# Performance work log

Hardware: AMD Instinct MI355X
Metric: run time of the kernel (lower is better)

Reference implementation:

```python
import jax, jax.numpy as jnp
import numpy as np

NUM_TOKENS = 8192
EMBED_DIM = 32
BETA = 1.0
DECAY = 0.99
L2_EPS = 1e-12  # torch F.normalize denom clamp


def l2norm(t):
    return t / jnp.maximum(jnp.linalg.norm(t, axis=-1, keepdims=True), L2_EPS)


def setup_inputs() -> dict:
    key = jax.random.key(0)
    k1, k2 = jax.random.split(key)
    z = jax.random.normal(k1, (32, EMBED_DIM, 16, 16), dtype=jnp.float32)  # [B, C, H, W]
    embedding = l2norm(jax.random.normal(k2, (NUM_TOKENS, EMBED_DIM), dtype=jnp.float32))
    cluster_sizes = jnp.zeros((NUM_TOKENS,), dtype=jnp.float32)
    return {"z": z, "embedding": embedding, "cluster_sizes": cluster_sizes}


def reference(z, embedding, cluster_sizes):
    B, C, H, W = z.shape
    zc = jnp.transpose(z, (0, 2, 3, 1))          # channel_last: [B, H, W, C]
    zn = l2norm(zc)
    z_flat = zn.reshape(-1, C)                   # [N, C], N = B*H*W

    # nearest centroid by cosine similarity (codebook rows are unit norm)
    cos_sim = z_flat @ embedding.T               # [N, K]
    token_ids = jnp.argmax(cos_sim, axis=-1)     # [N]
    z_q_flat = embedding[token_ids]              # gather, [N, C]
    z_q = z_q_flat.reshape(zn.shape)

    # EMA statistics (training branch; one-hot @ matmuls expressed as scatter-adds)
    bins = jnp.zeros((NUM_TOKENS,), z.dtype).at[token_ids].add(1.0)      # encodings.sum(0)
    new_cluster_sizes = cluster_sizes * DECAY + (1.0 - DECAY) * bins
    zero_mask = bins == 0
    bins_c = jnp.where(zero_mask, 1.0, bins)
    embed_sum = jnp.zeros((NUM_TOKENS, C), z.dtype).at[token_ids].add(z_flat)  # (z_flat.T @ onehot).T
    embed_normalized = l2norm(embed_sum / bins_c[:, None])
    embed_normalized = jnp.where(zero_mask[:, None], embedding, embed_normalized)
    new_embedding = l2norm(embedding * DECAY + (1.0 - DECAY) * embed_normalized)

    # commitment loss + straight-through estimator
    loss = BETA * jnp.mean((jax.lax.stop_gradient(z_q) - zn) ** 2)
    z_q_st = zn + jax.lax.stop_gradient(z_q - zn)
    z_q_out = jnp.transpose(z_q_st, (0, 3, 1, 2))  # back to [B, C, H, W]

    return (z_q_out, loss, token_ids.reshape(B, H, W), new_embedding, new_cluster_sizes)
```

## Files before the change

kernel.cpp:

```cpp
#include <hip/hip_runtime.h>


#define NTOK   8192
#define NCODE  8192
#define CDIM   32
#define HW     256
#define DECAYF 0.99f
#define EPSF   0.01f

#define OUT_ZQ   0
#define OUT_LOSS 262144
#define OUT_IDS  262145
#define OUT_EMB  270337
#define OUT_CS   532481

#define WS_ZN     0u
#define WS_ZNBF   1048576u
#define WS_EBF    1572864u
#define WS_PMAX   2097152u
#define WS_PACK   3145728u

#define CHUNK  256
#define NCHUNK (NCODE / CHUNK)
#define TILES  (CHUNK / 16)

typedef __attribute__((ext_vector_type(8))) short bf16x8;
typedef __attribute__((ext_vector_type(4))) float f32x4;

__device__ inline unsigned short f2bf(float x) {
    unsigned u = __float_as_uint(x);
    return (unsigned short)((u + 0x7FFFu + ((u >> 16) & 1u)) >> 16);
}
__device__ inline unsigned fmap(float s) {
    unsigned u = __float_as_uint(s);
    return (u & 0x80000000u) ? ~u : (u | 0x80000000u);
}

__device__ inline void stage_chunk(const unsigned short* __restrict__ ebf,
                                   int kbase, float4* lbs5, int t) {
    const float4* src = (const float4*)(ebf + (size_t)kbase * CDIM);
#pragma unroll
    for (int j = 0; j < 4; ++j) {
        int u = t + j * 256;
        int row = u >> 2, seg = u & 3;
        lbs5[row * 5 + seg] = src[u];
    }
}

__global__ __launch_bounds__(256) void k_prep(const float* __restrict__ z,
                                              const float* __restrict__ emb,
                                              float* __restrict__ zn,
                                              unsigned short* __restrict__ znbf,
                                              unsigned short* __restrict__ ebf,
                                              unsigned long long* __restrict__ packed,
                                              float* __restrict__ out) {
    int bid = blockIdx.x, t = threadIdx.x;
    if (bid < 32) {
        int n = bid * 256 + t;
        int b = n >> 8, hw = n & 255;
        const float* zp = z + (size_t)b * (CDIM * HW) + hw;
        float v[CDIM];
        float ss = 0.f;
#pragma unroll
        for (int c = 0; c < CDIM; ++c) {
            float tv = zp[c * HW];
            v[c] = tv;
            ss += tv * tv;
        }
        float d = fmaxf(sqrtf(ss), 1e-12f);
        float* o = zn + (size_t)n * CDIM;
        unsigned short* ob = znbf + (size_t)n * CDIM;
#pragma unroll
        for (int c = 0; c < CDIM; ++c) {
            float tv = v[c] / d;
            o[c] = tv;
            ob[c] = f2bf(tv);
        }
    } else if (bid < 160) {
        int base = (bid - 32) * 2048 + t * 8;
        const float4* s = (const float4*)(emb + base);
        float4 x4 = s[0], y4 = s[1];
        ushort4 u0 = {f2bf(x4.x), f2bf(x4.y), f2bf(x4.z), f2bf(x4.w)};
        ushort4 u1 = {f2bf(y4.x), f2bf(y4.y), f2bf(y4.z), f2bf(y4.w)};
        *(ushort4*)(ebf + base) = u0;
        *(ushort4*)(ebf + base + 4) = u1;
    } else if (bid < 164) {
        int base = (bid - 160) * 2048 + t;
#pragma unroll
        for (int j = 0; j < 8; ++j) packed[base + j * 256] = 0ull;
    } else {
        if (t == 0) out[OUT_LOSS] = 0.f;
    }
}

__global__ __launch_bounds__(256) void k_max(const unsigned short* __restrict__ znbf,
                                             const unsigned short* __restrict__ ebf,
                                             float* __restrict__ pmax) {
    __shared__ float4 lbs5[CHUNK * 5];
    __shared__ float lmax[256];
    int kbase = blockIdx.y * CHUNK;
    stage_chunk(ebf, kbase, lbs5, threadIdx.x);
    __syncthreads();

    int wave = threadIdx.x >> 6, lane = threadIdx.x & 63;
    int col = lane & 15, quad = lane >> 4;
    int wtok = blockIdx.x * 256 + wave * 64;

    bf16x8 a[4];
#pragma unroll
    for (int f = 0; f < 4; ++f)
        a[f] = *(const bf16x8*)(znbf + (size_t)(wtok + f * 16 + col) * CDIM + quad * 8);

    const bf16x8* bl = (const bf16x8*)lbs5;
    const f32x4 zero4 = {0.f, 0.f, 0.f, 0.f};
    float m[4][4];
#pragma unroll
    for (int f = 0; f < 4; ++f)
#pragma unroll
        for (int r = 0; r < 4; ++r) m[f][r] = -1e30f;

    for (int t = 0; t < TILES; ++t) {
        bf16x8 b = bl[(t * 16 + col) * 5 + quad];
#pragma unroll
        for (int f = 0; f < 4; ++f) {
            f32x4 d = __builtin_amdgcn_mfma_f32_16x16x32_bf16(a[f], b, zero4, 0, 0, 0);
#pragma unroll
            for (int r = 0; r < 4; ++r) m[f][r] = fmaxf(m[f][r], d[r]);
        }
    }
#pragma unroll
    for (int f = 0; f < 4; ++f)
#pragma unroll
        for (int r = 0; r < 4; ++r) {
            float v = m[f][r];
#pragma unroll
            for (int s = 1; s < 16; s <<= 1) v = fmaxf(v, __shfl_xor(v, s));
            if (col == 0) lmax[wave * 64 + f * 16 + quad * 4 + r] = v;
        }
    __syncthreads();
    pmax[(size_t)blockIdx.y * NTOK + blockIdx.x * 256 + threadIdx.x] = lmax[threadIdx.x];
}

__global__ __launch_bounds__(256) void k_pick(const unsigned short* __restrict__ znbf,
                                              const unsigned short* __restrict__ ebf,
                                              const float* __restrict__ zn,
                                              const float* __restrict__ emb,
                                              const float* __restrict__ pmax,
                                              unsigned long long* __restrict__ packed) {
    __shared__ float4 lbs5[CHUNK * 5];
    __shared__ float lthr[256];
    int kbase = blockIdx.y * CHUNK;
    stage_chunk(ebf, kbase, lbs5, threadIdx.x);
    {
        int tok = blockIdx.x * 256 + threadIdx.x;
        float mx = -1e30f;
#pragma unroll
        for (int ch = 0; ch < NCHUNK; ++ch)
            mx = fmaxf(mx, pmax[(size_t)ch * NTOK + tok]);
        lthr[threadIdx.x] = mx - EPSF;
    }
    __syncthreads();

    int wave = threadIdx.x >> 6, lane = threadIdx.x & 63;
    int col = lane & 15, quad = lane >> 4;
    int wtok = blockIdx.x * 256 + wave * 64;

    bf16x8 a[4];
#pragma unroll
    for (int f = 0; f < 4; ++f)
        a[f] = *(const bf16x8*)(znbf + (size_t)(wtok + f * 16 + col) * CDIM + quad * 8);

    float thr[4][4];
#pragma unroll
    for (int f = 0; f < 4; ++f)
#pragma unroll
        for (int r = 0; r < 4; ++r)
            thr[f][r] = lthr[wave * 64 + f * 16 + quad * 4 + r];

    const bf16x8* bl = (const bf16x8*)lbs5;
    const f32x4 zero4 = {0.f, 0.f, 0.f, 0.f};

    for (int t = 0; t < TILES; ++t) {
        bf16x8 b = bl[(t * 16 + col) * 5 + quad];
#pragma unroll
        for (int f = 0; f < 4; ++f) {
            f32x4 d = __builtin_amdgcn_mfma_f32_16x16x32_bf16(a[f], b, zero4, 0, 0, 0);
#pragma unroll
            for (int r = 0; r < 4; ++r) {
                if (d[r] >= thr[f][r]) {
                    int tok = wtok + f * 16 + quad * 4 + r;
                    int code = kbase + t * 16 + col;
                    const float* zp = zn + (size_t)tok * CDIM;
                    const float* ep = emb + (size_t)code * CDIM;
                    float a0 = 0.f, a1 = 0.f, a2 = 0.f, a3 = 0.f;
#pragma unroll
                    for (int j = 0; j < 8; ++j) {
                        a0 = __builtin_fmaf(zp[4 * j + 0], ep[4 * j + 0], a0);
                        a1 = __builtin_fmaf(zp[4 * j + 1], ep[4 * j + 1], a1);
                        a2 = __builtin_fmaf(zp[4 * j + 2], ep[4 * j + 2], a2);
                        a3 = __builtin_fmaf(zp[4 * j + 3], ep[4 * j + 3], a3);
                    }
                    float s = (a0 + a1) + (a2 + a3);
                    atomicMax(packed + tok, ((unsigned long long)fmap(s) << 13) |
                                            (unsigned long long)(8191 - code));
                }
            }
        }
    }
}

__global__ __launch_bounds__(256) void k_final(const unsigned long long* __restrict__ packed,
                                               const float* __restrict__ zn,
                                               const float* __restrict__ emb,
                                               const float* __restrict__ cs,
                                               float* __restrict__ out) {
    __shared__ float lesum[32][32];
    __shared__ int lbins[32];
    __shared__ int lsid[32];
    __shared__ float ls4[4];

    int blk = blockIdx.x, t = threadIdx.x;
    int wave = t >> 6, lane = t & 63;
    int tok0 = blk * 32, kbase = blk * 32;

    if (t < 32) lbins[t] = 0;
#pragma unroll
    for (int i = 0; i < 4; ++i) {
        int idx = i * 256 + t;
        lesum[idx >> 5][idx & 31] = 0.f;
    }
    if (t < 32) {
        int n = tok0 + t;
        int id = 8191 - (int)(packed[n] & 8191ull);
        lsid[t] = id;
        out[OUT_IDS + n] = (float)id;
    }
    __syncthreads();

    float s = 0.f;
#pragma unroll
    for (int i = 0; i < 4; ++i) {
        int idx = i * 256 + t;
        int tl = idx >> 5, c = idx & 31;
        int n = tok0 + tl;
        int id = lsid[tl];
        float ev = emb[(size_t)id * CDIM + c];
        float zv = zn[(size_t)n * CDIM + c];
        int b = n >> 8, hw = n & 255;
        out[OUT_ZQ + ((size_t)b * CDIM + c) * HW + hw] = ev;
        float dd = ev - zv;
        s += dd * dd;
    }
#pragma unroll
    for (int off = 32; off > 0; off >>= 1) s += __shfl_down(s, off);
    if (lane == 0) ls4[wave] = s;
    __syncthreads();
    if (t == 0)
        atomicAdd(out + OUT_LOSS,
                  (ls4[0] + ls4[1] + ls4[2] + ls4[3]) * (1.0f / 262144.0f));

    for (int i = 0; i < 32; ++i) {
        int n = i * 256 + t;
        int id = 8191 - (int)(packed[n] & 8191ull);
        unsigned kl = (unsigned)(id - kbase);
        if (kl < 32u) {
            atomicAdd(&lbins[kl], 1);
            const float* zp = zn + (size_t)n * CDIM;
#pragma unroll
            for (int c = 0; c < CDIM; ++c)
                atomicAdd(&lesum[kl][c], zp[c]);
        }
    }
    __syncthreads();

#pragma unroll
    for (int i = 0; i < 4; ++i) {
        int idx = i * 256 + t;
        int kl = idx >> 5, c = idx & 31;
        int k = kbase + kl;
        int bi = lbins[kl];
        float bf = (float)bi;
        bool zero = (bi == 0);
        float tv = lesum[kl][c] / (zero ? 1.0f : bf);
        float ss = tv * tv;
#pragma unroll
        for (int sh = 1; sh < 32; sh <<= 1) ss += __shfl_xor(ss, sh);
        float d = fmaxf(sqrtf(ss), 1e-12f);
        float ew = emb[(size_t)k * CDIM + c];
        float en = zero ? ew : (tv / d);
        float w = ew * DECAYF + (1.0f - DECAYF) * en;
        float ss2 = w * w;
#pragma unroll
        for (int sh = 1; sh < 32; sh <<= 1) ss2 += __shfl_xor(ss2, sh);
        float d2 = fmaxf(sqrtf(ss2), 1e-12f);
        out[OUT_EMB + (size_t)k * CDIM + c] = w / d2;
        if (c == 0) out[OUT_CS + k] = cs[k] * DECAYF + (1.0f - DECAYF) * bf;
    }
}

extern "C" void kernel_launch(void* const* d_in, const int* in_sizes, int n_in,
                              void* d_out, int out_size, void* d_ws, size_t ws_size,
                              hipStream_t stream) {
    const float* z   = (const float*)d_in[0];
    const float* emb = (const float*)d_in[1];
    const float* cs  = (const float*)d_in[2];
    float* out = (float*)d_out;
    char* ws = (char*)d_ws;

    float* zn                  = (float*)(ws + WS_ZN);
    unsigned short* znbf       = (unsigned short*)(ws + WS_ZNBF);
    unsigned short* ebf        = (unsigned short*)(ws + WS_EBF);
    float* pmax                = (float*)(ws + WS_PMAX);
    unsigned long long* packed = (unsigned long long*)(ws + WS_PACK);

    k_prep<<<dim3(165), 256, 0, stream>>>(z, emb, zn, znbf, ebf, packed, out);
    k_max<<<dim3(NTOK / 256, NCHUNK), 256, 0, stream>>>(znbf, ebf, pmax);
    k_pick<<<dim3(NTOK / 256, NCHUNK), 256, 0, stream>>>(znbf, ebf, zn, emb, pmax, packed);
    k_final<<<dim3(256), 256, 0, stream>>>(packed, zn, emb, cs, out);
}
```

Before: 120.2 us.

## Rewrite pick kernel to rescore only tokens whose chunk max is near global max

```diff
diff --git a/kernel.cpp b/kernel.cpp
--- a/kernel.cpp
+++ b/kernel.cpp
@@ -141,71 +141,64 @@
     pmax[(size_t)blockIdx.y * NTOK + blockIdx.x * 256 + threadIdx.x] = lmax[threadIdx.x];
 }
 
-__global__ __launch_bounds__(256) void k_pick(const unsigned short* __restrict__ znbf,
-                                              const unsigned short* __restrict__ ebf,
-                                              const float* __restrict__ zn,
-                                              const float* __restrict__ emb,
-                                              const float* __restrict__ pmax,
-                                              unsigned long long* __restrict__ packed) {
-    __shared__ float4 lbs5[CHUNK * 5];
-    __shared__ float lthr[256];
-    int kbase = blockIdx.y * CHUNK;
-    stage_chunk(ebf, kbase, lbs5, threadIdx.x);
-    {
-        int tok = blockIdx.x * 256 + threadIdx.x;
-        float mx = -1e30f;
-#pragma unroll
-        for (int ch = 0; ch < NCHUNK; ++ch)
-            mx = fmaxf(mx, pmax[(size_t)ch * NTOK + tok]);
-        lthr[threadIdx.x] = mx - EPSF;
-    }
-    __syncthreads();
-
-    int wave = threadIdx.x >> 6, lane = threadIdx.x & 63;
-    int col = lane & 15, quad = lane >> 4;
-    int wtok = blockIdx.x * 256 + wave * 64;
-
-    bf16x8 a[4];
-#pragma unroll
-    for (int f = 0; f < 4; ++f)
-        a[f] = *(const bf16x8*)(znbf + (size_t)(wtok + f * 16 + col) * CDIM + quad * 8);
-
-    float thr[4][4];
-#pragma unroll
-    for (int f = 0; f < 4; ++f)
-#pragma unroll
-        for (int r = 0; r < 4; ++r)
-            thr[f][r] = lthr[wave * 64 + f * 16 + quad * 4 + r];
-
-    const bf16x8* bl = (const bf16x8*)lbs5;
-    const f32x4 zero4 = {0.f, 0.f, 0.f, 0.f};
-
-    for (int t = 0; t < TILES; ++t) {
-        bf16x8 b = bl[(t * 16 + col) * 5 + quad];
-#pragma unroll
-        for (int f = 0; f < 4; ++f) {
-            f32x4 d = __builtin_amdgcn_mfma_f32_16x16x32_bf16(a[f], b, zero4, 0, 0, 0);
-#pragma unroll
-            for (int r = 0; r < 4; ++r) {
-                if (d[r] >= thr[f][r]) {
-                    int tok = wtok + f * 16 + quad * 4 + r;
-                    int code = kbase + t * 16 + col;
-                    const float* zp = zn + (size_t)tok * CDIM;
-                    const float* ep = emb + (size_t)code * CDIM;
-                    float a0 = 0.f, a1 = 0.f, a2 = 0.f, a3 = 0.f;
-#pragma unroll
-                    for (int j = 0; j < 8; ++j) {
-                        a0 = __builtin_fmaf(zp[4 * j + 0], ep[4 * j + 0], a0);
-                        a1 = __builtin_fmaf(zp[4 * j + 1], ep[4 * j + 1], a1);
-                        a2 = __builtin_fmaf(zp[4 * j + 2], ep[4 * j + 2], a2);
-                        a3 = __builtin_fmaf(zp[4 * j + 3], ep[4 * j + 3], a3);
-                    }
-                    float s = (a0 + a1) + (a2 + a3);
-                    atomicMax(packed + tok, ((unsigned long long)fmap(s) << 13) |
-                                            (unsigned long long)(8191 - code));
-                }
-            }
-        }
+__global__ __launch_bounds__(256, 4) void k_pick(const float* __restrict__ zn,
+                                                 const float* __restrict__ emb,
+                                                 const float* __restrict__ pmax,
+                                                 unsigned long long* __restrict__ packed) {
+    __shared__ int qlist[256];
+    __shared__ int qcnt;
+    int t = threadIdx.x, lane = t & 63;
+    int x = blockIdx.x, y = blockIdx.y;
+    int code = y * CHUNK + t;
+
+    if (t == 0) qcnt = 0;
+
+    const float4* ef = (const float4*)(emb + (size_t)code * CDIM);
+    float4 e0 = ef[0], e1 = ef[1], e2 = ef[2], e3 = ef[3];
+    float4 e4 = ef[4], e5 = ef[5], e6 = ef[6], e7 = ef[7];
+
+    int tok = x * 256 + t;
+    float mx = -1e30f, pmy = -1e30f;
+#pragma unroll
+    for (int ch = 0; ch < NCHUNK; ++ch) {
+        float p = pmax[(size_t)ch * NTOK + tok];
+        if (ch == y) pmy = p;
+        mx = fmaxf(mx, p);
+    }
+    __syncthreads();
+    if (pmy >= mx - EPSF) qlist[atomicAdd(&qcnt, 1)] = t;
+    __syncthreads();
+    int nq = qcnt;
+
+    for (int i = 0; i < nq; ++i) {
+        int tl = __builtin_amdgcn_readfirstlane(qlist[i]);
+        int n = x * 256 + tl;
+        const float* zp = zn + (size_t)n * CDIM;
+        float a0 = zp[0] * e0.x, a1 = zp[1] * e0.y;
+        float a2 = zp[2] * e0.z, a3 = zp[3] * e0.w;
+        a0 = __builtin_fmaf(zp[4], e1.x, a0);  a1 = __builtin_fmaf(zp[5], e1.y, a1);
+        a2 = __builtin_fmaf(zp[6], e1.z, a2);  a3 = __builtin_fmaf(zp[7], e1.w, a3);
+        a0 = __builtin_fmaf(zp[8], e2.x, a0);  a1 = __builtin_fmaf(zp[9], e2.y, a1);
+        a2 = __builtin_fmaf(zp[10], e2.z, a2); a3 = __builtin_fmaf(zp[11], e2.w, a3);
+        a0 = __builtin_fmaf(zp[12], e3.x, a0); a1 = __builtin_fmaf(zp[13], e3.y, a1);
+        a2 = __builtin_fmaf(zp[14], e3.z, a2); a3 = __builtin_fmaf(zp[15], e3.w, a3);
+        a0 = __builtin_fmaf(zp[16], e4.x, a0); a1 = __builtin_fmaf(zp[17], e4.y, a1);
+        a2 = __builtin_fmaf(zp[18], e4.z, a2); a3 = __builtin_fmaf(zp[19], e4.w, a3);
+        a0 = __builtin_fmaf(zp[20], e5.x, a0); a1 = __builtin_fmaf(zp[21], e5.y, a1);
+        a2 = __builtin_fmaf(zp[22], e5.z, a2); a3 = __builtin_fmaf(zp[23], e5.w, a3);
+        a0 = __builtin_fmaf(zp[24], e6.x, a0); a1 = __builtin_fmaf(zp[25], e6.y, a1);
+        a2 = __builtin_fmaf(zp[26], e6.z, a2); a3 = __builtin_fmaf(zp[27], e6.w, a3);
+        a0 = __builtin_fmaf(zp[28], e7.x, a0); a1 = __builtin_fmaf(zp[29], e7.y, a1);
+        a2 = __builtin_fmaf(zp[30], e7.z, a2); a3 = __builtin_fmaf(zp[31], e7.w, a3);
+        float s = (a0 + a1) + (a2 + a3);
+        unsigned long long key = ((unsigned long long)fmap(s) << 13) |
+                                 (unsigned long long)(8191 - code);
+#pragma unroll
+        for (int sh = 1; sh < 64; sh <<= 1) {
+            unsigned long long o = __shfl_xor(key, sh);
+            if (o > key) key = o;
+        }
+        if (lane == 0) atomicMax(packed + n, key);
     }
 }
 
@@ -315,6 +308,6 @@
 
     k_prep<<<dim3(165), 256, 0, stream>>>(z, emb, zn, znbf, ebf, packed, out);
     k_max<<<dim3(NTOK / 256, NCHUNK), 256, 0, stream>>>(znbf, ebf, pmax);
-    k_pick<<<dim3(NTOK / 256, NCHUNK), 256, 0, stream>>>(znbf, ebf, zn, emb, pmax, packed);
+    k_pick<<<dim3(NTOK / 256, NCHUNK), 256, 0, stream>>>(zn, emb, pmax, packed);
     k_final<<<dim3(256), 256, 0, stream>>>(packed, zn, emb, cs, out);
 }
```

After: 123.8 us. +3.0%, slower.
